# Performance work log

Hardware: AMD Instinct MI355X
Metric: run time of the kernel (lower is better)

The kernel has to match this reference:

```python
import jax, jax.numpy as jnp
import numpy as np

B, S, DIM = 2, 2048, 2048
NH, NKV, HD = 32, 8, 64
N_REP = NH // NKV


def apply_rope(x, cos, sin):
    # x: (B, H, S, HD); cos/sin: (S, HD//2)
    d = x.shape[-1] // 2
    x1, x2 = x[..., :d], x[..., d:]
    c = cos[None, None, :, :]
    s = sin[None, None, :, :]
    return jnp.concatenate([x1 * c - x2 * s, x2 * c + x1 * s], axis=-1)


def setup_inputs() -> dict:
    key = jax.random.key(0)
    ks = jax.random.split(key, 8)
    x = jax.random.normal(ks[0], (B, S, DIM), dtype=jnp.float32)
    # plausible RoPE tables
    inv_freq = 1.0 / (10000.0 ** (jnp.arange(0, HD, 2, dtype=jnp.float32) / HD))
    t = jnp.arange(S, dtype=jnp.float32)
    freqs = jnp.outer(t, inv_freq)  # (S, HD//2)
    rope_cos = jnp.cos(freqs)
    rope_sin = jnp.sin(freqs)
    doc_ids = jnp.sort(jax.random.randint(ks[1], (B, S), 0, 8, dtype=jnp.int32), axis=-1)
    std = 0.02
    Wq = jax.random.normal(ks[2], (NH * HD, DIM), dtype=jnp.float32) * std
    Wk = jax.random.normal(ks[3], (NKV * HD, DIM), dtype=jnp.float32) * std
    Wv = jax.random.normal(ks[4], (NKV * HD, DIM), dtype=jnp.float32) * std
    Wo = jax.random.normal(ks[5], (DIM, NH * HD), dtype=jnp.float32) * std
    return {"x": x, "rope_cos": rope_cos, "rope_sin": rope_sin,
            "doc_ids": doc_ids, "Wq": Wq, "Wk": Wk, "Wv": Wv, "Wo": Wo}


def reference(x, rope_cos, rope_sin, doc_ids, Wq, Wk, Wv, Wo):
    batch, seq_len, _ = x.shape
    q = (x @ Wq.T).reshape(batch, seq_len, NH, HD).transpose(0, 2, 1, 3)   # (B,NH,S,HD)
    k = (x @ Wk.T).reshape(batch, seq_len, NKV, HD).transpose(0, 2, 1, 3)  # (B,NKV,S,HD)
    v = (x @ Wv.T).reshape(batch, seq_len, NKV, HD).transpose(0, 2, 1, 3)

    q = apply_rope(q, rope_cos, rope_sin)
    k = apply_rope(k, rope_cos, rope_sin)

    # GQA expansion (repeat_interleave on head dim)
    k = jnp.repeat(k, N_REP, axis=1)  # (B,NH,S,HD)
    v = jnp.repeat(v, N_REP, axis=1)

    # block-diagonal causal mask from packed doc ids
    doc_mask = doc_ids[:, :, None] == doc_ids[:, None, :]          # (B,S,S)
    causal = jnp.tril(jnp.ones((seq_len, seq_len), dtype=bool))    # (S,S)
    mask = (doc_mask & causal[None])[:, None, :, :]                # (B,1,S,S)

    scale = 1.0 / jnp.sqrt(jnp.asarray(HD, dtype=q.dtype))
    scores = jnp.einsum("bhqd,bhkd->bhqk", q, k) * scale
    scores = jnp.where(mask, scores, jnp.finfo(scores.dtype).min)
    attn = jax.nn.softmax(scores, axis=-1)
    out = jnp.einsum("bhqk,bhkd->bhqd", attn, v)                   # (B,NH,S,HD)
    out = out.transpose(0, 2, 1, 3).reshape(batch, seq_len, NH * HD)
    return out @ Wo.T
```

## Files before the change

### kernel.cpp

```cpp
#include <hip/hip_runtime.h>
#include <hip/hip_bf16.h>

#define BB   2
#define SEQ  2048
#define DIMD 2048
#define NHH  32
#define NKVV 8
#define HDD  64
#define QKVS 3072

typedef __bf16 bf16x8 __attribute__((ext_vector_type(8)));
typedef float  floatx4 __attribute__((ext_vector_type(4)));

typedef __attribute__((address_space(1))) const void* gas_ptr;
typedef __attribute__((address_space(3))) void*       las_ptr;

#define MFMA16 __builtin_amdgcn_mfma_f32_16x16x32_bf16
#define CBAR() asm volatile("" ::: "memory")

__device__ __forceinline__ unsigned short f2bu(float f) {
    __hip_bfloat16 h = __float2bfloat16(f);
    return *reinterpret_cast<unsigned short*>(&h);
}

#define C_X  (8u  * 1024 * 1024)
#define C_WQ (4u  * 1024 * 1024)
#define C_WK (1u  * 1024 * 1024)
#define C_WV (1u  * 1024 * 1024)
#define C_WO (4u  * 1024 * 1024)
__global__ void cvt_all(const float* __restrict__ x,  const float* __restrict__ wq,
                        const float* __restrict__ wk, const float* __restrict__ wv,
                        const float* __restrict__ wo,
                        __hip_bfloat16* __restrict__ xb,
                        __hip_bfloat16* __restrict__ wqkv,
                        __hip_bfloat16* __restrict__ wob)
{
    unsigned i = (blockIdx.x * blockDim.x + threadIdx.x) * 4;
    const float* src; __hip_bfloat16* dst;
    if (i < C_X)                       { src = x  + i;                    dst = xb + i; }
    else if (i < C_X + C_WQ)           { unsigned o = i - C_X;            src = wq + o; dst = wqkv + o; }
    else if (i < C_X + C_WQ + C_WK)    { unsigned o = i - C_X - C_WQ;     src = wk + o; dst = wqkv + C_WQ + o; }
    else if (i < C_X + C_WQ + C_WK + C_WV) { unsigned o = i - C_X - C_WQ - C_WK; src = wv + o; dst = wqkv + C_WQ + C_WK + o; }
    else                               { unsigned o = i - C_X - C_WQ - C_WK - C_WV; if (o >= C_WO) return; src = wo + o; dst = wob + o; }
    float4 v = *reinterpret_cast<const float4*>(src);
    dst[0] = __float2bfloat16(v.x);
    dst[1] = __float2bfloat16(v.y);
    dst[2] = __float2bfloat16(v.z);
    dst[3] = __float2bfloat16(v.w);
}

template <typename OutT, bool ROPE, int BN>
__global__ __launch_bounds__(512, 2) void gemm8p(
    const __hip_bfloat16* __restrict__ Abf,
    const __hip_bfloat16* __restrict__ Wbf,
    OutT* __restrict__ C,
    int M, int N, int K, int ldc,
    const float* __restrict__ cosb, const float* __restrict__ sinb)
{
    constexpr int  NF = BN / 64;
    constexpr int  WN = BN / 4;
    constexpr bool B2 = (BN == 256);
    constexpr int  HB = (BN / 2) * 64;

    const __bf16* Ag = reinterpret_cast<const __bf16*>(Abf);
    const __bf16* Wg = reinterpret_cast<const __bf16*>(Wbf);

    __shared__ __align__(16) __bf16 As[2][256 * 64];
    __shared__ __align__(16) __bf16 Bs[2][BN * 64];

    const int NT   = K >> 6;
    const int tid  = threadIdx.x;
    const int wid  = tid >> 6;
    const int lane = tid & 63;
    const int l15  = lane & 15;
    const int l4   = lane >> 4;
    const int wm   = wid >> 2;
    const int wn   = wid & 3;

    const int gx   = M >> 8;
    const int nwg  = (int)gridDim.x;
    const int orig = (int)blockIdx.x;
    const int wg   = (orig & 7) * (nwg >> 3) + (orig >> 3);
    const int bm   = (wg % gx) << 8;
    const int bn   = (wg / gx) * BN;

    const int r0 = tid >> 3;
    const int c0 = ((tid & 7) ^ (r0 & 7)) * 8;
    const __bf16* aS00 = Ag + (size_t)(bm + r0) * K + c0;
    const __bf16* aS01 = aS00 + (size_t)64  * K;
    const __bf16* aS10 = aS00 + (size_t)128 * K;
    const __bf16* aS11 = aS00 + (size_t)192 * K;
    const __bf16* bS00 = Wg + (size_t)(bn + r0) * K + c0;
    const __bf16* bS01 = bS00 + (size_t)64 * K;
    const __bf16* bS10 = bS00 + (size_t)(BN / 2) * K;
    const __bf16* bS11 = bS10 + (size_t)64 * K;

    bf16x8 af[4][2], b01[2][2], b23[2][2];
    floatx4 acc[8][NF] = {};

    auto stage2 = [&](const __bf16* s0, const __bf16* s1, __bf16* d, int kt) {
        int k0 = (kt < NT ? kt : NT - 1) << 6;
        __builtin_amdgcn_global_load_lds((gas_ptr)(s0 + k0), (las_ptr)(d + tid * 8), 16, 0, 0);
        if (s1)
        __builtin_amdgcn_global_load_lds((gas_ptr)(s1 + k0), (las_ptr)(d + 4096 + tid * 8), 16, 0, 0);
    };
    auto lda = [&](int buf, int mbase) {
        #pragma unroll
        for (int mi = 0; mi < 4; ++mi)
            #pragma unroll
            for (int kk = 0; kk < 2; ++kk) {
                int row = wm * 128 + (mbase + mi) * 16 + l15;
                int ch  = ((kk * 4 + l4) ^ (row & 7)) * 8;
                af[mi][kk] = *reinterpret_cast<const bf16x8*>(&As[buf][row * 64 + ch]);
            }
    };
    auto ldb = [&](int buf, bf16x8 (&regs)[2][2], int nbase) {
        #pragma unroll
        for (int ni = 0; ni < 2; ++ni)
            #pragma unroll
            for (int kk = 0; kk < 2; ++kk) {
                int row = wn * WN + (nbase + ni) * 16 + l15;
                int ch  = ((kk * 4 + l4) ^ (row & 7)) * 8;
                regs[ni][kk] = *reinterpret_cast<const bf16x8*>(&Bs[buf][row * 64 + ch]);
            }
    };
    auto mmBoth = [&](int mbase, bf16x8 (&bregs)[2][2], int nb) {
        #pragma unroll
        for (int mi = 0; mi < 4; ++mi)
            #pragma unroll
            for (int ni = 0; ni < 2; ++ni) {
                acc[mbase + mi][nb + ni] = MFMA16(af[mi][0], bregs[ni][0], acc[mbase + mi][nb + ni], 0, 0, 0);
                acc[mbase + mi][nb + ni] = MFMA16(af[mi][1], bregs[ni][1], acc[mbase + mi][nb + ni], 0, 0, 0);
            }
    };
    auto mmOne = [&](int mbase, int kk) {
        #pragma unroll
        for (int mi = 0; mi < 4; ++mi)
            #pragma unroll
            for (int ni = 0; ni < 2; ++ni)
                acc[mbase + mi][ni] = MFMA16(af[mi][kk], b01[ni][kk], acc[mbase + mi][ni], 0, 0, 0);
    };

    auto ktile = [&](int cur, int t) {
        lda(cur, 0);
        ldb(cur, b01, 0);
        stage2(aS10, aS11, &As[cur ^ 1][8192], t + 1);
        CBAR(); __builtin_amdgcn_s_barrier(); CBAR();
        asm volatile("s_waitcnt lgkmcnt(0)" ::: "memory");
        __builtin_amdgcn_sched_barrier(0);
        __builtin_amdgcn_s_setprio(1);
        if constexpr (B2) mmBoth(0, b01, 0); else mmOne(0, 0);
        __builtin_amdgcn_s_setprio(0);
        CBAR(); __builtin_amdgcn_s_barrier(); CBAR();
        if constexpr (B2) ldb(cur, b23, 2);
        stage2(bS00, B2 ? bS01 : (const __bf16*)nullptr, &Bs[cur ^ 1][0], t + 1);
        CBAR(); __builtin_amdgcn_s_barrier(); CBAR();
        asm volatile("s_waitcnt lgkmcnt(0)" ::: "memory");
        __builtin_amdgcn_sched_barrier(0);
        __builtin_amdgcn_s_setprio(1);
        if constexpr (B2) mmBoth(0, b23, 2); else mmOne(0, 1);
        __builtin_amdgcn_s_setprio(0);
        CBAR(); __builtin_amdgcn_s_barrier(); CBAR();
        lda(cur, 4);
        stage2(bS10, B2 ? bS11 : (const __bf16*)nullptr, &Bs[cur ^ 1][HB], t + 1);
        CBAR(); __builtin_amdgcn_s_barrier(); CBAR();
        asm volatile("s_waitcnt lgkmcnt(0)" ::: "memory");
        __builtin_amdgcn_sched_barrier(0);
        __builtin_amdgcn_s_setprio(1);
        if constexpr (B2) mmBoth(4, b23, 2); else mmOne(4, 1);
        __builtin_amdgcn_s_setprio(0);
        CBAR(); __builtin_amdgcn_s_barrier(); CBAR();
        stage2(aS00, aS01, &As[cur][0], t + 2);
        CBAR(); __builtin_amdgcn_s_barrier(); CBAR();
        __builtin_amdgcn_s_setprio(1);
        if constexpr (B2) mmBoth(4, b01, 0); else mmOne(4, 0);
        __builtin_amdgcn_s_setprio(0);
        asm volatile("s_waitcnt vmcnt(2)" ::: "memory");
        CBAR(); __builtin_amdgcn_s_barrier(); CBAR();
    };

    stage2(aS00, aS01, &As[0][0],    0);
    stage2(aS10, aS11, &As[0][8192], 0);
    stage2(bS00, B2 ? bS01 : (const __bf16*)nullptr, &Bs[0][0],  0);
    stage2(bS10, B2 ? bS11 : (const __bf16*)nullptr, &Bs[0][HB], 0);
    stage2(aS00, aS01, &As[1][0],    1);
    asm volatile("s_waitcnt vmcnt(2)" ::: "memory");
    CBAR(); __builtin_amdgcn_s_barrier(); CBAR();

    #pragma unroll 1
    for (int t = 0; t < NT; t += 2) {
        ktile(0, t);
        ktile(1, t + 1);
    }

    if constexpr (ROPE) {
        bool do_rope = (bn + wn * 64) < 2560;
        #pragma unroll
        for (int mi = 0; mi < 8; ++mi) {
            #pragma unroll
            for (int r = 0; r < 4; ++r) {
                int row = bm + wm * 128 + mi * 16 + l4 * 4 + r;
                int s   = row & (SEQ - 1);
                #pragma unroll
                for (int j = 0; j < 2; ++j) {
                    float x1 = acc[mi][j][r], x2 = acc[mi][j + 2][r];
                    if (do_rope) {
                        float cf = cosb[s * 32 + j * 16 + l15];
                        float sf = sinb[s * 32 + j * 16 + l15];
                        float o1 = x1 * cf - x2 * sf;
                        float o2 = x2 * cf + x1 * sf;
                        x1 = o1; x2 = o2;
                    }
                    int col = bn + wn * 64 + j * 16 + l15;
                    C[(size_t)row * ldc + col]      = __float2bfloat16(x1);
                    C[(size_t)row * ldc + col + 32] = __float2bfloat16(x2);
                }
            }
        }
    } else {
        #pragma unroll
        for (int mi = 0; mi < 8; ++mi)
            #pragma unroll
            for (int ni = 0; ni < NF; ++ni)
                #pragma unroll
                for (int r = 0; r < 4; ++r) {
                    int row = bm + wm * 128 + mi * 16 + l4 * 4 + r;
                    int col = bn + wn * WN + ni * 16 + l15;
                    if constexpr (sizeof(OutT) == 4)
                        C[(size_t)row * ldc + col] = acc[mi][ni][r];
                    else
                        C[(size_t)row * ldc + col] = __float2bfloat16(acc[mi][ni][r]);
                }
    }
}

__global__ void transpose_v(const __hip_bfloat16* __restrict__ qkv,
                            unsigned short* __restrict__ vT)
{
    __shared__ unsigned short T[64][68];
    int s0  = blockIdx.x * 64;
    int kvh = blockIdx.y;
    int b   = blockIdx.z;
    int tid = threadIdx.x;

    int srow = tid >> 2, dg = (tid & 3) * 16;
    const unsigned short* src = reinterpret_cast<const unsigned short*>(qkv)
        + (size_t)(b * SEQ + s0 + srow) * QKVS + 2560 + kvh * 64 + dg;
    #pragma unroll
    for (int i = 0; i < 4; ++i)
        *reinterpret_cast<ushort4*>(&T[srow][dg + i * 4]) =
            *reinterpret_cast<const ushort4*>(src + i * 4);
    __syncthreads();

    int drow = tid >> 2, sg = (tid & 3) * 16;
    unsigned short* dst = vT + ((size_t)(b * NKVV + kvh) * 64 + drow) * SEQ + s0 + sg;
    #pragma unroll
    for (int i = 0; i < 4; ++i) {
        ushort4 u;
        u.x = T[sg + i * 4 + 0][drow];
        u.y = T[sg + i * 4 + 1][drow];
        u.z = T[sg + i * 4 + 2][drow];
        u.w = T[sg + i * 4 + 3][drow];
        *reinterpret_cast<ushort4*>(dst + i * 4) = u;
    }
}

__global__ __launch_bounds__(256) void attn_mfma(
    const __hip_bfloat16* __restrict__ qkv,
    const unsigned short* __restrict__ vT,
    const int* __restrict__ doc,
    __hip_bfloat16* __restrict__ ob)
{
    int qblk = (int)gridDim.x - 1 - (int)blockIdx.x;
    int h    = blockIdx.y;
    int b    = blockIdx.z;
    int kvh  = h >> 2;
    int tid  = threadIdx.x;
    int wv   = tid >> 6;
    int lane = tid & 63;
    int l15  = lane & 15;
    int l4   = lane >> 4;
    int q0   = qblk * 128;
    int qw   = q0 + wv * 32;

    __shared__ unsigned short Ks[64 * 64];
    __shared__ unsigned short Vts[64 * 64];
    __shared__ unsigned short Pb[4][32][76];
    __shared__ int kdoc[64];

    const unsigned short* qus = reinterpret_cast<const unsigned short*>(qkv);
    const unsigned short* kus = qus + 2048;

    bf16x8 aq[2][2];
    #pragma unroll
    for (int qt = 0; qt < 2; ++qt) {
        const unsigned short* qrow = qus + (size_t)(b * SEQ + qw + qt * 16 + l15) * QKVS + h * HDD;
        aq[qt][0] = *reinterpret_cast<const bf16x8*>(qrow + l4 * 8);
        aq[qt][1] = *reinterpret_cast<const bf16x8*>(qrow + 32 + l4 * 8);
    }
    int qd[2][4];
    #pragma unroll
    for (int qt = 0; qt < 2; ++qt)
        #pragma unroll
        for (int r = 0; r < 4; ++r)
            qd[qt][r] = doc[b * SEQ + qw + qt * 16 + l4 * 4 + r];
    int qd_w   = doc[b * SEQ + qw];
    int qd_blk = doc[b * SEQ + q0];

    float mrow[2][4], lrow[2][4];
    #pragma unroll
    for (int qt = 0; qt < 2; ++qt)
        #pragma unroll
        for (int r = 0; r < 4; ++r) { mrow[qt][r] = -1e30f; lrow[qt][r] = 0.f; }
    floatx4 accO[2][4] = {};

    int slot0 = tid, slot1 = tid + 256;
    int row0 = slot0 >> 3, g0 = (slot0 & 7) ^ (row0 & 7);
    int row1 = slot1 >> 3, g1 = (slot1 & 7) ^ (row1 & 7);
    const unsigned short* vtb = vT + ((size_t)(b * NKVV + kvh) * 64) * SEQ;

    int kc_end = 2 * qblk + 1;
    for (int kc = 0; kc <= kc_end; ++kc) {
        int k0 = kc * 64;
        int kd_last = doc[b * SEQ + k0 + 63];
        if (kd_last < qd_blk) continue;

        __syncthreads();
        __builtin_amdgcn_global_load_lds(
            (gas_ptr)(kus + (size_t)(b * SEQ + k0 + row0) * QKVS + kvh * HDD + g0 * 8),
            (las_ptr)(Ks + slot0 * 8), 16, 0, 0);
        __builtin_amdgcn_global_load_lds(
            (gas_ptr)(kus + (size_t)(b * SEQ + k0 + row1) * QKVS + kvh * HDD + g1 * 8),
            (las_ptr)(Ks + slot1 * 8), 16, 0, 0);
        __builtin_amdgcn_global_load_lds(
            (gas_ptr)(vtb + (size_t)row0 * SEQ + k0 + g0 * 8),
            (las_ptr)(Vts + slot0 * 8), 16, 0, 0);
        __builtin_amdgcn_global_load_lds(
            (gas_ptr)(vtb + (size_t)row1 * SEQ + k0 + g1 * 8),
            (las_ptr)(Vts + slot1 * 8), 16, 0, 0);
        if (tid < 64) kdoc[tid] = doc[b * SEQ + k0 + tid];
        __syncthreads();

        if (k0 <= qw + 31 && kd_last >= qd_w) {
            #pragma unroll
            for (int qt = 0; qt < 2; ++qt) {
                float s[4][4];
                #pragma unroll
                for (int t = 0; t < 4; ++t) {
                    int krow = t * 16 + l15;
                    bf16x8 bk0 = *reinterpret_cast<const bf16x8*>(Ks + krow * 64 + ((l4 ^ (krow & 7)) * 8));
                    bf16x8 bk1 = *reinterpret_cast<const bf16x8*>(Ks + krow * 64 + ((((l4 + 4)) ^ (krow & 7)) * 8));
                    floatx4 acc = {};
                    acc = MFMA16(aq[qt][0], bk0, acc, 0, 0, 0);
                    acc = MFMA16(aq[qt][1], bk1, acc, 0, 0, 0);
                    int key = k0 + krow;
                    int kd  = kdoc[krow];
                    #pragma unroll
                    for (int r = 0; r < 4; ++r) {
                        int qrow = qw + qt * 16 + l4 * 4 + r;
                        bool valid = (kd == qd[qt][r]) && (key <= qrow);
                        s[t][r] = valid ? acc[r] * 0.125f : -1e30f;
                    }
                }
                #pragma unroll
                for (int r = 0; r < 4; ++r) {
                    float pm = fmaxf(fmaxf(s[0][r], s[1][r]), fmaxf(s[2][r], s[3][r]));
                    pm = fmaxf(pm, __shfl_xor(pm, 1));
                    pm = fmaxf(pm, __shfl_xor(pm, 2));
                    pm = fmaxf(pm, __shfl_xor(pm, 4));
                    pm = fmaxf(pm, __shfl_xor(pm, 8));
                    float mnew = fmaxf(mrow[qt][r], pm);
                    float alpha = __expf(mrow[qt][r] - mnew);
                    mrow[qt][r] = mnew;
                    float ps = 0.f;
                    #pragma unroll
                    for (int t = 0; t < 4; ++t) {
                        float p = (s[t][r] <= -1e29f) ? 0.f : __expf(s[t][r] - mnew);
                        Pb[wv][qt * 16 + l4 * 4 + r][t * 16 + l15] = f2bu(p);
                        ps += p;
                    }
                    ps += __shfl_xor(ps, 1);
                    ps += __shfl_xor(ps, 2);
                    ps += __shfl_xor(ps, 4);
                    ps += __shfl_xor(ps, 8);
                    lrow[qt][r] = lrow[qt][r] * alpha + ps;
                    #pragma unroll
                    for (int t = 0; t < 4; ++t) accO[qt][t][r] *= alpha;
                }
            }
            #pragma unroll
            for (int qt = 0; qt < 2; ++qt) {
                bf16x8 ap0 = *reinterpret_cast<const bf16x8*>(&Pb[wv][qt * 16 + l15][l4 * 8]);
                bf16x8 ap1 = *reinterpret_cast<const bf16x8*>(&Pb[wv][qt * 16 + l15][32 + l4 * 8]);
                #pragma unroll
                for (int t = 0; t < 4; ++t) {
                    int vrow = t * 16 + l15;
                    bf16x8 bv0 = *reinterpret_cast<const bf16x8*>(Vts + vrow * 64 + ((l4 ^ (vrow & 7)) * 8));
                    bf16x8 bv1 = *reinterpret_cast<const bf16x8*>(Vts + vrow * 64 + ((((l4 + 4)) ^ (vrow & 7)) * 8));
                    accO[qt][t] = MFMA16(ap0, bv0, accO[qt][t], 0, 0, 0);
                    accO[qt][t] = MFMA16(ap1, bv1, accO[qt][t], 0, 0, 0);
                }
            }
        }
    }

    #pragma unroll
    for (int qt = 0; qt < 2; ++qt)
        #pragma unroll
        for (int r = 0; r < 4; ++r) {
            float inv = 1.0f / lrow[qt][r];
            size_t base = (size_t)(b * SEQ + qw + qt * 16 + l4 * 4 + r) * (NHH * HDD) + h * HDD;
            #pragma unroll
            for (int t = 0; t < 4; ++t)
                ob[base + t * 16 + l15] = __float2bfloat16(accO[qt][t][r] * inv);
        }
}

extern "C" void kernel_launch(void* const* d_in, const int* in_sizes, int n_in,
                              void* d_out, int out_size, void* d_ws, size_t ws_size,
                              hipStream_t stream) {
    const float* x  = (const float*)d_in[0];
    const float* rc = (const float*)d_in[1];
    const float* rs = (const float*)d_in[2];
    const int*   dc = (const int*)d_in[3];
    const float* Wq = (const float*)d_in[4];
    const float* Wk = (const float*)d_in[5];
    const float* Wv = (const float*)d_in[6];
    const float* Wo = (const float*)d_in[7];
    float* out = (float*)d_out;

    const int M    = BB * SEQ;
    const int KVD  = NKVV * HDD;
    const int QKVN = DIMD + 2 * KVD;

    char* ws = (char*)d_ws;
    size_t off = 0;
    auto alloc = [&](size_t elems) { __hip_bfloat16* p = (__hip_bfloat16*)(ws + off); off += elems * 2; return p; };
    __hip_bfloat16* xb   = alloc((size_t)M * DIMD);
    __hip_bfloat16* wqkv = alloc((size_t)QKVN * DIMD);
    __hip_bfloat16* wob  = alloc((size_t)DIMD * DIMD);
    __hip_bfloat16* qkv  = alloc((size_t)M * QKVN);
    __hip_bfloat16* abuf = alloc((size_t)M * DIMD);
    unsigned short* vtb  = (unsigned short*)alloc((size_t)BB * NKVV * HDD * SEQ);

    {
        unsigned total4 = (C_X + C_WQ + C_WK + C_WV + C_WO) / 4;
        cvt_all<<<dim3((total4 + 255) / 256), 256, 0, stream>>>(
            x, Wq, Wk, Wv, Wo, xb, wqkv, wob);
    }

    gemm8p<__hip_bfloat16, true, 256><<<dim3((M / 256) * (QKVN / 256)), 512, 0, stream>>>(
        xb, wqkv, qkv, M, QKVN, DIMD, QKVN, rc, rs);

    transpose_v<<<dim3(SEQ / 64, NKVV, BB), 256, 0, stream>>>(qkv, vtb);

    attn_mfma<<<dim3(SEQ / 128, NHH, BB), 256, 0, stream>>>(qkv, vtb, dc, abuf);

    gemm8p<float, false, 128><<<dim3((M / 256) * (DIMD / 128)), 512, 0, stream>>>(
        abuf, wob, out, M, DIMD, DIMD, DIMD, nullptr, nullptr);
}
```

Baseline: 298.3 us.

## Reorganize GEMM LDS tiles into interleaved quadrants with finer vmcnt waits

Splits the A and B shared-memory tiles into interleaved quadrants: rows 0-63 and 128-191 form one A half, and B rows alternate in 32/16-row groups into even and odd halves. Each k-tile is computed as four quadrant MFMA blocks, and the staging order and s_waitcnt vmcnt counts are adjusted so each global->LDS load is waited on only just before its buffer is reused. The aim is to overlap loads with compute more evenly and to drop the full vmcnt drain near the tail. In exchange the vmcnt bookkeeping becomes fragile, and a wrong count could cause races.

```diff
diff --git a/kernel.cpp b/kernel.cpp
--- a/kernel.cpp
+++ b/kernel.cpp
@@ -60,7 +60,7 @@
     constexpr int  NF = BN / 64;
     constexpr int  WN = BN / 4;
     constexpr bool B2 = (BN == 256);
-    constexpr int  HB = (BN / 2) * 64;
+    constexpr int  NB = B2 ? 2 : 1;
 
     const __bf16* Ag = reinterpret_cast<const __bf16*>(Abf);
     const __bf16* Wg = reinterpret_cast<const __bf16*>(Wbf);
@@ -86,105 +86,121 @@
 
     const int r0 = tid >> 3;
     const int c0 = ((tid & 7) ^ (r0 & 7)) * 8;
-    const __bf16* aS00 = Ag + (size_t)(bm + r0) * K + c0;
-    const __bf16* aS01 = aS00 + (size_t)64  * K;
-    const __bf16* aS10 = aS00 + (size_t)128 * K;
-    const __bf16* aS11 = aS00 + (size_t)192 * K;
-    const __bf16* bS00 = Wg + (size_t)(bn + r0) * K + c0;
-    const __bf16* bS01 = bS00 + (size_t)64 * K;
-    const __bf16* bS10 = bS00 + (size_t)(BN / 2) * K;
-    const __bf16* bS11 = bS10 + (size_t)64 * K;
-
-    bf16x8 af[4][2], b01[2][2], b23[2][2];
+    const __bf16* aAL0 = Ag + (size_t)(bm + r0) * K + c0;
+    const __bf16* aAL1 = aAL0 + (size_t)128 * K;
+    const __bf16* aAH0 = aAL0 + (size_t)64  * K;
+    const __bf16* aAH1 = aAL0 + (size_t)192 * K;
+    const __bf16* bBE0; const __bf16* bBE1 = nullptr;
+    const __bf16* bBO0; const __bf16* bBO1 = nullptr;
+    if constexpr (B2) {
+        int rBE = ((r0 >> 5) << 6) + (r0 & 31);
+        bBE0 = Wg + (size_t)(bn + rBE) * K + c0;
+        bBE1 = bBE0 + (size_t)128 * K;
+        bBO0 = bBE0 + (size_t)32  * K;
+        bBO1 = bBO0 + (size_t)128 * K;
+    } else {
+        int rBE = ((r0 >> 4) << 5) + (r0 & 15);
+        bBE0 = Wg + (size_t)(bn + rBE) * K + c0;
+        bBO0 = bBE0 + (size_t)16 * K;
+    }
+
+    bf16x8 af[4][2];
+    bf16x8 bq[2][2][2];
     floatx4 acc[8][NF] = {};
 
+    auto stage1 = [&](const __bf16* s, __bf16* d, int kt) {
+        int k0 = (kt < NT ? kt : NT - 1) << 6;
+        __builtin_amdgcn_global_load_lds((gas_ptr)(s + k0), (las_ptr)(d + tid * 8), 16, 0, 0);
+    };
     auto stage2 = [&](const __bf16* s0, const __bf16* s1, __bf16* d, int kt) {
         int k0 = (kt < NT ? kt : NT - 1) << 6;
         __builtin_amdgcn_global_load_lds((gas_ptr)(s0 + k0), (las_ptr)(d + tid * 8), 16, 0, 0);
-        if (s1)
         __builtin_amdgcn_global_load_lds((gas_ptr)(s1 + k0), (las_ptr)(d + 4096 + tid * 8), 16, 0, 0);
     };
-    auto lda = [&](int buf, int mbase) {
+    auto lda = [&](int buf, int qm) {
         #pragma unroll
         for (int mi = 0; mi < 4; ++mi)
             #pragma unroll
             for (int kk = 0; kk < 2; ++kk) {
-                int row = wm * 128 + (mbase + mi) * 16 + l15;
-                int ch  = ((kk * 4 + l4) ^ (row & 7)) * 8;
-                af[mi][kk] = *reinterpret_cast<const bf16x8*>(&As[buf][row * 64 + ch]);
-            }
-    };
-    auto ldb = [&](int buf, bf16x8 (&regs)[2][2], int nbase) {
-        #pragma unroll
-        for (int ni = 0; ni < 2; ++ni)
+                int pos = wm * 64 + mi * 16 + l15;
+                int ch  = ((kk * 4 + l4) ^ (pos & 7)) * 8;
+                af[mi][kk] = *reinterpret_cast<const bf16x8*>(&As[buf][qm * 8192 + pos * 64 + ch]);
+            }
+    };
+    auto ldb = [&](int buf, int qn) {
+        if constexpr (B2) {
+            #pragma unroll
+            for (int ni = 0; ni < 2; ++ni)
+                #pragma unroll
+                for (int kk = 0; kk < 2; ++kk) {
+                    int pos = wn * 32 + ni * 16 + l15;
+                    int ch  = ((kk * 4 + l4) ^ (pos & 7)) * 8;
+                    bq[qn][ni][kk] = *reinterpret_cast<const bf16x8*>(&Bs[buf][qn * 8192 + pos * 64 + ch]);
+                }
+        } else {
             #pragma unroll
             for (int kk = 0; kk < 2; ++kk) {
-                int row = wn * WN + (nbase + ni) * 16 + l15;
-                int ch  = ((kk * 4 + l4) ^ (row & 7)) * 8;
-                regs[ni][kk] = *reinterpret_cast<const bf16x8*>(&Bs[buf][row * 64 + ch]);
-            }
-    };
-    auto mmBoth = [&](int mbase, bf16x8 (&bregs)[2][2], int nb) {
+                int pos = wn * 16 + l15;
+                int ch  = ((kk * 4 + l4) ^ (pos & 7)) * 8;
+                bq[qn][0][kk] = *reinterpret_cast<const bf16x8*>(&Bs[buf][qn * 4096 + pos * 64 + ch]);
+            }
+        }
+    };
+    auto mmQuad = [&](int qm, int qn) {
         #pragma unroll
         for (int mi = 0; mi < 4; ++mi)
             #pragma unroll
-            for (int ni = 0; ni < 2; ++ni) {
-                acc[mbase + mi][nb + ni] = MFMA16(af[mi][0], bregs[ni][0], acc[mbase + mi][nb + ni], 0, 0, 0);
-                acc[mbase + mi][nb + ni] = MFMA16(af[mi][1], bregs[ni][1], acc[mbase + mi][nb + ni], 0, 0, 0);
-            }
-    };
-    auto mmOne = [&](int mbase, int kk) {
-        #pragma unroll
-        for (int mi = 0; mi < 4; ++mi)
-            #pragma unroll
-            for (int ni = 0; ni < 2; ++ni)
-                acc[mbase + mi][ni] = MFMA16(af[mi][kk], b01[ni][kk], acc[mbase + mi][ni], 0, 0, 0);
+            for (int ni = 0; ni < NB; ++ni) {
+                floatx4& a = acc[qm * 4 + mi][qn * NB + ni];
+                a = MFMA16(af[mi][0], bq[qn][ni][0], a, 0, 0, 0);
+                a = MFMA16(af[mi][1], bq[qn][ni][1], a, 0, 0, 0);
+            }
     };
 
     auto ktile = [&](int cur, int t) {
-        lda(cur, 0);
-        ldb(cur, b01, 0);
-        stage2(aS10, aS11, &As[cur ^ 1][8192], t + 1);
+        int nxt = cur ^ 1;
+        lda(cur, 0); ldb(cur, 0);
+        if constexpr (B2) stage2(bBE0, bBE1, &Bs[nxt][0], t + 1);
+        else              stage1(bBE0,       &Bs[nxt][0], t + 1);
         CBAR(); __builtin_amdgcn_s_barrier(); CBAR();
         asm volatile("s_waitcnt lgkmcnt(0)" ::: "memory");
         __builtin_amdgcn_sched_barrier(0);
-        __builtin_amdgcn_s_setprio(1);
-        if constexpr (B2) mmBoth(0, b01, 0); else mmOne(0, 0);
-        __builtin_amdgcn_s_setprio(0);
-        CBAR(); __builtin_amdgcn_s_barrier(); CBAR();
-        if constexpr (B2) ldb(cur, b23, 2);
-        stage2(bS00, B2 ? bS01 : (const __bf16*)nullptr, &Bs[cur ^ 1][0], t + 1);
+        __builtin_amdgcn_s_setprio(1); mmQuad(0, 0); __builtin_amdgcn_s_setprio(0);
+        if constexpr (B2) asm volatile("s_waitcnt vmcnt(6)" ::: "memory");
+        else              asm volatile("s_waitcnt vmcnt(5)" ::: "memory");
+        CBAR(); __builtin_amdgcn_s_barrier(); CBAR();
+        ldb(cur, 1);
+        if constexpr (B2) stage2(bBO0, bBO1, &Bs[nxt][8192], t + 1);
+        else              stage1(bBO0,       &Bs[nxt][4096], t + 1);
         CBAR(); __builtin_amdgcn_s_barrier(); CBAR();
         asm volatile("s_waitcnt lgkmcnt(0)" ::: "memory");
         __builtin_amdgcn_sched_barrier(0);
-        __builtin_amdgcn_s_setprio(1);
-        if constexpr (B2) mmBoth(0, b23, 2); else mmOne(0, 1);
-        __builtin_amdgcn_s_setprio(0);
-        CBAR(); __builtin_amdgcn_s_barrier(); CBAR();
-        lda(cur, 4);
-        stage2(bS10, B2 ? bS11 : (const __bf16*)nullptr, &Bs[cur ^ 1][HB], t + 1);
+        __builtin_amdgcn_s_setprio(1); mmQuad(0, 1); __builtin_amdgcn_s_setprio(0);
+        if constexpr (B2) asm volatile("s_waitcnt vmcnt(6)" ::: "memory");
+        else              asm volatile("s_waitcnt vmcnt(4)" ::: "memory");
+        CBAR(); __builtin_amdgcn_s_barrier(); CBAR();
+        lda(cur, 1);
+        stage2(aAH0, aAH1, &As[nxt][8192], t + 1);
         CBAR(); __builtin_amdgcn_s_barrier(); CBAR();
         asm volatile("s_waitcnt lgkmcnt(0)" ::: "memory");
         __builtin_amdgcn_sched_barrier(0);
-        __builtin_amdgcn_s_setprio(1);
-        if constexpr (B2) mmBoth(4, b23, 2); else mmOne(4, 1);
-        __builtin_amdgcn_s_setprio(0);
-        CBAR(); __builtin_amdgcn_s_barrier(); CBAR();
-        stage2(aS00, aS01, &As[cur][0], t + 2);
-        CBAR(); __builtin_amdgcn_s_barrier(); CBAR();
-        __builtin_amdgcn_s_setprio(1);
-        if constexpr (B2) mmBoth(4, b01, 0); else mmOne(4, 0);
-        __builtin_amdgcn_s_setprio(0);
-        asm volatile("s_waitcnt vmcnt(2)" ::: "memory");
-        CBAR(); __builtin_amdgcn_s_barrier(); CBAR();
-    };
-
-    stage2(aS00, aS01, &As[0][0],    0);
-    stage2(aS10, aS11, &As[0][8192], 0);
-    stage2(bS00, B2 ? bS01 : (const __bf16*)nullptr, &Bs[0][0],  0);
-    stage2(bS10, B2 ? bS11 : (const __bf16*)nullptr, &Bs[0][HB], 0);
-    stage2(aS00, aS01, &As[1][0],    1);
-    asm volatile("s_waitcnt vmcnt(2)" ::: "memory");
+        __builtin_amdgcn_s_setprio(1); mmQuad(1, 1); __builtin_amdgcn_s_setprio(0);
+        CBAR(); __builtin_amdgcn_s_barrier(); CBAR();
+        stage2(aAL0, aAL1, &As[cur][0], t + 2);
+        CBAR(); __builtin_amdgcn_s_barrier(); CBAR();
+        __builtin_amdgcn_s_setprio(1); mmQuad(1, 0); __builtin_amdgcn_s_setprio(0);
+        if constexpr (B2) asm volatile("s_waitcnt vmcnt(6)" ::: "memory");
+        else              asm volatile("s_waitcnt vmcnt(5)" ::: "memory");
+        CBAR(); __builtin_amdgcn_s_barrier(); CBAR();
+    };
+
+    stage2(aAL0, aAL1, &As[0][0], 0);
+    if constexpr (B2) { stage2(bBE0, bBE1, &Bs[0][0], 0);    stage2(bBO0, bBO1, &Bs[0][8192], 0); }
+    else              { stage1(bBE0, &Bs[0][0], 0);          stage1(bBO0, &Bs[0][4096], 0); }
+    stage2(aAH0, aAH1, &As[0][8192], 0);
+    stage2(aAL0, aAL1, &As[1][0], 1);
+    if constexpr (B2) asm volatile("s_waitcnt vmcnt(6)" ::: "memory");
+    else              asm volatile("s_waitcnt vmcnt(5)" ::: "memory");
     CBAR(); __builtin_amdgcn_s_barrier(); CBAR();
 
     #pragma unroll 1
```

Result: no change. 300.2 us (+0.6%).
